# Kernel tuning notes

Measured on AMD Instinct MI355X. Metric: run time of the kernel, lower is better.

The kernel has to match this reference:

```python
import jax, jax.numpy as jnp
import numpy as np

NEG_SLOPE = 0.2
EPS = 1e-6
K = 16


def vec_lna(x, Wf, Wd):
    # x: (B, Cin, 3, ...). Vector-neuron linear + VN-LeakyReLU.
    p = jnp.einsum('oc,bc...->bo...', Wf, x)          # features (B, Cout, 3, ...)
    d = jnp.einsum('oc,bc...->bo...', Wd, x)          # directions (B, Cd, 3, ...), Cd=Cout or 1 (shared)
    dot = jnp.sum(p * d, axis=2, keepdims=True)
    dsq = jnp.sum(d * d, axis=2, keepdims=True)
    p_ref = p - (dot / (dsq + EPS)) * d               # reflect negative part onto hyperplane
    return NEG_SLOPE * p + (1.0 - NEG_SLOPE) * jnp.where(dot >= 0, p, p_ref)


def knn_idx_fn(pts, k):
    # pts: (B, N, 3) -> (B, N, k) indices of k nearest neighbors (incl. self)
    sq = jnp.sum(pts * pts, axis=-1)                  # (B, N)
    d2 = sq[:, :, None] + sq[:, None, :] - 2.0 * jnp.einsum('bnd,bmd->bnm', pts, pts)
    _, idx = jax.lax.top_k(-d2, k)                    # smallest distances
    return idx


def graph_feature(x, idx):
    # x: (B, C, 3, N), idx: (B, N, k) -> (B, 2C, 3, N, k)
    nb = jax.vmap(lambda xb, ib: xb[:, :, ib])(x, idx)  # (B, C, 3, N, k)
    xc = x[..., None]
    return jnp.concatenate([nb - xc, jnp.broadcast_to(xc, nb.shape)], axis=1)


def _winit(key, co, ci):
    return jax.random.normal(key, (co, ci), dtype=jnp.float32) * np.sqrt(2.0 / ci).astype(np.float32)


def setup_inputs() -> dict:
    key = jax.random.key(0)
    ks = jax.random.split(key, 16)
    B, N = 4, 2048
    x = jax.random.normal(ks[0], (B, 3, N), dtype=jnp.float32)
    return {
        'x': x,
        'w1f': _winit(ks[1], 16, 2),   'w1d': _winit(ks[2], 16, 2),
        'w2f': _winit(ks[3], 32, 32),  'w2d': _winit(ks[4], 32, 32),
        'w3f': _winit(ks[5], 64, 64),  'w3d': _winit(ks[6], 64, 64),
        'w4f': _winit(ks[7], 128, 128),'w4d': _winit(ks[8], 128, 128),
        'wcf': _winit(ks[9], 128, 240),'wcd': _winit(ks[10], 1, 240),   # shared nonlinearity -> 1 dir channel
        'wi1f': _winit(ks[11], 128, 256), 'wi1d': _winit(ks[12], 128, 256),
        'wi2f': _winit(ks[13], 256, 128), 'wi2d': _winit(ks[14], 256, 128),
    }


def reference(x, w1f, w1d, w2f, w2d, w3f, w3d, w4f, w4d, wcf, wcd, wi1f, wi1d, wi2f, wi2d):
    # x: (B, 3, N)
    pts = jnp.transpose(x, (0, 2, 1))                 # (B, N, 3)
    idx = knn_idx_fn(pts, K)                          # (B, N, K) -- fixed graph (use_dg=False)
    h = x[:, None]                                    # (B, 1, 3, N)
    h = vec_lna(graph_feature(h, idx), w1f, w1d)
    x1 = h.mean(axis=-1)                              # (B, 16, 3, N)
    h = vec_lna(graph_feature(x1, idx), w2f, w2d)
    x2 = h.mean(axis=-1)                              # (B, 32, 3, N)
    h = vec_lna(graph_feature(x2, idx), w3f, w3d)
    x3 = h.mean(axis=-1)                              # (B, 64, 3, N)
    h = vec_lna(graph_feature(x3, idx), w4f, w4d)
    x4 = h.mean(axis=-1)                              # (B, 128, 3, N)
    xc = vec_lna(jnp.concatenate([x1, x2, x3, x4], axis=1), wcf, wcd)  # (B, 128, 3, N)
    xm = jnp.broadcast_to(xc.mean(axis=-1, keepdims=True), xc.shape)
    xcat = jnp.concatenate([xc, xm], axis=1)          # (B, 256, 3, N)
    x0 = vec_lna(vec_lna(xcat, wi1f, wi1d), wi2f, wi2d)
    inv = jnp.sum(xcat * x0, axis=2)                  # (B, 256, N) rotation-invariant features
    return inv
```

## Files before the change

kernel.cpp:

```cpp
#include <hip/hip_runtime.h>
#include <hip/hip_fp16.h>

#define NPTS  2048
#define BATCH 4
#define NBP   8192
#define MROWS 24576
#define KNN_K 16

typedef short bf16x8 __attribute__((ext_vector_type(8)));
typedef float f32x4  __attribute__((ext_vector_type(4)));

static __device__ __forceinline__ void split_bf16(float a, unsigned short& h, unsigned short& l)
{
    unsigned u = __float_as_uint(a);
    unsigned hr = (u + 0x7FFFu + ((u >> 16) & 1u)) & 0xFFFF0000u;
    h = (unsigned short)(hr >> 16);
    float rem = a - __uint_as_float(hr);
    unsigned v = __float_as_uint(rem);
    l = (unsigned short)((v + 0x7FFFu + ((v >> 16) & 1u)) >> 16);
}

static __device__ __forceinline__ float bf2(unsigned short h, unsigned short l)
{
    return __uint_as_float((unsigned)h << 16) + __uint_as_float((unsigned)l << 16);
}

static __device__ __forceinline__ float lna_scale(float dot, float dsq)
{
    return (dot < 0.f) ? 0.8f * dot * __builtin_amdgcn_rcpf(dsq + 1e-6f) : 0.f;
}

static __device__ __forceinline__ unsigned long long shfl_xor_u64(unsigned long long v, int mask)
{
    unsigned lo = (unsigned)v, hi = (unsigned)(v >> 32);
    lo = (unsigned)__shfl_xor((int)lo, mask, 64);
    hi = (unsigned)__shfl_xor((int)hi, mask, 64);
    return ((unsigned long long)hi << 32) | lo;
}

static __device__ __forceinline__ int xcd_swizzle(int i, int G)
{
    int batch  = (i >> 1) & 3;
    int within = ((i >> 3) << 1) | (i & 1);
    return batch * (G >> 2) + within;
}

static __device__ __forceinline__ float wbig_val(const float* __restrict__ Wf,
                                                 const float* __restrict__ Wd,
                                                 int j, int c, int O, int C)
{
    if (j < 2 * O) {
        int o = j >> 1;
        return (j & 1) ? Wd[o * 2 * C + c] : Wf[o * 2 * C + c];
    }
    int o = (j - 2 * O) >> 1;
    return (j & 1) ? (Wd[o * 2 * C + C + c] - Wd[o * 2 * C + c])
                   : (Wf[o * 2 * C + C + c] - Wf[o * 2 * C + c]);
}

static __device__ __forceinline__ int frag_ix(int r, int c, int RB)
{
    return (((c >> 5) * RB + (r >> 4)) * 64 + ((c >> 3) & 3) * 16 + (r & 15)) * 8 + (c & 7);
}

#define PC0 1572864
#define PC1 (PC0 + 4096)
#define PC2 (PC1 + 8192)
#define PC3 (PC2 + 32768)
#define PC4 (PC3 + 49152)
#define PC5 (PC4 + 65536)
#define PC6 (PC5 + 65536)
#define KNN_BLOCKS (NBP / 4)
#define PREP_BLOCKS (PC6 / 256)

__global__ __launch_bounds__(256) void prep_knn_kernel(
    const float* __restrict__ x, int* __restrict__ idx,
    __half* __restrict__ AH, float* __restrict__ AG,
    const float* __restrict__ w1f, const float* __restrict__ w1d,
    const float* __restrict__ w2f, const float* __restrict__ w2d,
    unsigned short* __restrict__ Wb2h, unsigned short* __restrict__ Wb2l,
    const float* __restrict__ w3f, const float* __restrict__ w3d,
    unsigned short* __restrict__ Wb3h, unsigned short* __restrict__ Wb3l,
    const float* __restrict__ w4f, const float* __restrict__ w4d,
    unsigned short* __restrict__ Wb4h, unsigned short* __restrict__ Wb4l,
    const float* __restrict__ wcf, const float* __restrict__ wcd,
    unsigned short* __restrict__ Wch, unsigned short* __restrict__ Wcl,
    const float* __restrict__ wi1f, const float* __restrict__ wi1d,
    unsigned short* __restrict__ Wi1h, unsigned short* __restrict__ Wi1l,
    const float* __restrict__ wi2f, const float* __restrict__ wi2d,
    unsigned short* __restrict__ Wi2h, unsigned short* __restrict__ Wi2l)
{
    __shared__ unsigned ksh[4][64 * 34];
    if (blockIdx.x < KNN_BLOCKS) {
        const int t  = threadIdx.x & 63;
        const int wq = threadIdx.x >> 6;
        const int bn = blockIdx.x * 4 + wq;
        const int b = bn >> 11;
        const int n = bn & (NPTS - 1);
        const float* xb = x + b * 3 * NPTS;
        const float qx = xb[n], qy = xb[NPTS + n], qz = xb[2 * NPTS + n];
        const float sqn = fmaf(qz, qz, fmaf(qy, qy, qx * qx));
        unsigned* ks = &ksh[wq][t * 34];

        unsigned gm[4];
        int ga[4];
#pragma unroll
        for (int g = 0; g < 4; g++) {
            unsigned kk[8];
#pragma unroll
            for (int j = 0; j < 8; j++) {
                const int i = g * 8 + j;
                const int m = (i << 6) + t;
                float mx = xb[m], my = xb[NPTS + m], mz = xb[2 * NPTS + m];
                float sqm = fmaf(mz, mz, fmaf(my, my, mx * mx));
                float dt  = fmaf(qz, mz, fmaf(qy, my, qx * mx));
                float d2  = sqn + sqm - 2.0f * dt;
                unsigned u = __float_as_uint(d2);
                u ^= (u & 0x80000000u) ? 0xFFFFFFFFu : 0x80000000u;
                kk[j] = u;
            }
            *(uint2*)&ks[g * 8 + 0] = make_uint2(kk[0], kk[1]);
            *(uint2*)&ks[g * 8 + 2] = make_uint2(kk[2], kk[3]);
            *(uint2*)&ks[g * 8 + 4] = make_uint2(kk[4], kk[5]);
            *(uint2*)&ks[g * 8 + 6] = make_uint2(kk[6], kk[7]);
            unsigned bg = kk[0];
            int ba = g * 8;
#pragma unroll
            for (int j = 1; j < 8; j++) {
                if (kk[j] < bg) { bg = kk[j]; ba = g * 8 + j; }
            }
            gm[g] = bg; ga[g] = ba;
        }
        unsigned lm = gm[0];
        int il = ga[0];
#pragma unroll
        for (int g = 1; g < 4; g++) if (gm[g] < lm) { lm = gm[g]; il = ga[g]; }

        unsigned long long pk = ((unsigned long long)lm << 32) | (unsigned)((il << 6) | t);
        int res = -1;
        for (int r = 0; r < KNN_K; r++) {
            unsigned long long w = pk;
#pragma unroll
            for (int off = 32; off > 0; off >>= 1) {
                unsigned long long o = shfl_xor_u64(w, off);
                w = (o < w) ? o : w;
            }
            if (t == r) res = (int)(w & 0xFFFFFFFFull);

            if (pk == w) {
                ks[il] = 0xFFFFFFFFu;
                const int g = il >> 3;
                unsigned bg = ks[g * 8];
                int ba = g * 8;
#pragma unroll
                for (int j = 1; j < 8; j++) {
                    unsigned kv = ks[g * 8 + j];
                    if (kv < bg) { bg = kv; ba = g * 8 + j; }
                }
                gm[g] = bg; ga[g] = ba;
                lm = gm[0]; il = ga[0];
#pragma unroll
                for (int g2 = 1; g2 < 4; g2++) if (gm[g2] < lm) { lm = gm[g2]; il = ga[g2]; }
                pk = ((unsigned long long)lm << 32) | (unsigned)((il << 6) | t);
            }
        }
        if (t < KNN_K) idx[bn * KNN_K + t] = res;
        return;
    }

    const int i = (blockIdx.x - KNN_BLOCKS) * 256 + threadIdx.x;
    if (i < PC0) {
        int o = i & 63;
        int row = i >> 6;
        int v = row % 3;
        int gp = row / 3;
        int b = gp >> 11;
        int n = gp & (NPTS - 1);
        float xv = x[(b * 3 + v) * NPTS + n];
        float wv = wbig_val(w1f, w1d, o, 0, 16, 1);
        float val = xv * wv;
        if (o < 32) AH[(size_t)row * 32 + o] = __float2half(val);
        else        AG[(size_t)row * 32 + o - 32] = val;
    } else if (i < PC6) {
        float v = 0.f;
        unsigned short *ph, *pl;
        int ix;
        if (i < PC1) {
            ix = i - PC0;
            int c = ix & 31, j = ix >> 5;
            if (c < 16) v = wbig_val(w2f, w2d, j, c, 32, 16);
            ph = Wb2h; pl = Wb2l;
        } else if (i < PC2) {
            ix = i - PC1;
            int c = ix & 31, j = ix >> 5;
            v = wbig_val(w3f, w3d, j, c, 64, 32);
            ph = Wb3h; pl = Wb3l;
        } else if (i < PC3) {
            ix = i - PC2;
            int c = ix & 63, j = ix >> 6;
            v = wbig_val(w4f, w4d, j, c, 128, 64);
            ph = Wb4h; pl = Wb4l;
        } else if (i < PC4) {
            ix = i - PC3;
            int c = ix & 255, r = ix >> 8;
            if (c < 240) {
                if (r < 128) v = wcf[r * 240 + c];
                else if (r < 129) v = wcd[(r - 128) * 240 + c];
            }
            ph = Wch; pl = Wcl;
            ix = frag_ix(r, c, 12);
        } else if (i < PC5) {
            ix = i - PC4;
            int c = ix & 255, r = ix >> 8;
            if (r < 128) v = wi1f[r * 256 + c];
            else v = wi1d[(r - 128) * 256 + c];
            ph = Wi1h; pl = Wi1l;
        } else {
            ix = i - PC5;
            int c = ix & 127, r = ix >> 7;
            int o = r >> 1;
            v = (r & 1) ? wi2d[o * 128 + c] : wi2f[o * 128 + c];
            ph = Wi2h; pl = Wi2l;
            ix = frag_ix(r, c, 32);
        }
        unsigned short h, l;
        split_bf16(v, h, l);
        ph[ix] = h; pl[ix] = l;
    }
}

template <int OIN, int NF>
__global__ __launch_bounds__(256, 3) void edge_gemm_kernel(
    const __half* __restrict__ AHin, const float* __restrict__ AGin,
    const int* __restrict__ idx,
    unsigned short* __restrict__ X240h, unsigned short* __restrict__ X240l, int ooff,
    const unsigned short* __restrict__ Wh, const unsigned short* __restrict__ Wl,
    __half* __restrict__ OUTA, float* __restrict__ OUTG)
{
    constexpr int PTS = 16;
    constexpr int NC = NF * 64;
    constexpr int twoO = NC / 2;
    constexpr int LDW = 40;
    constexpr int CPT = OIN / 16;
    constexpr int twoOin = 2 * OIN;

    __shared__ unsigned short Xsh[48][32];
    __shared__ unsigned short Xsl[48][32];
    __shared__ unsigned short wbh[NC][LDW];
    __shared__ unsigned short wbl[NC][LDW];
    __shared__ int sIdx[PTS][KNN_K];

    const int lb = xcd_swizzle(blockIdx.x, gridDim.x);
    const int tid = threadIdx.x;

    for (int rr = tid; rr < NC; rr += 256) {
#pragma unroll
        for (int scc = 0; scc < 4; scc++) {
            *(uint4*)&wbh[rr][scc * 8] = *(const uint4*)(Wh + (size_t)rr * 32 + scc * 8);
            *(uint4*)&wbl[rr][scc * 8] = *(const uint4*)(Wl + (size_t)rr * 32 + scc * 8);
        }
    }
    for (int j = tid; j < PTS * KNN_K; j += 256)
        sIdx[j >> 4][j & 15] = idx[(lb * PTS + (j >> 4)) * KNN_K + (j & 15)];
    __syncthreads();

    const int op = tid & 15;
    const int pt = tid >> 4;
    const int gp = lb * PTS + pt;
    const int b = gp >> 11;
    const int rown = gp * 3;
    const int bbase = (b << 11) * 3;

    float cg[3][2 * CPT];
#pragma unroll
    for (int v = 0; v < 3; v++) {
        if constexpr (CPT == 2) {
            float4 c4 = *(const float4*)&AGin[(size_t)(rown + v) * twoOin + 4 * op];
            cg[v][0] = c4.x; cg[v][1] = c4.y; cg[v][2] = c4.z; cg[v][3] = c4.w;
        } else {
            float2 c2 = *(const float2*)&AGin[(size_t)(rown + v) * twoOin + 2 * op];
            cg[v][0] = c2.x; cg[v][1] = c2.y;
        }
    }
    float am[CPT][3];
#pragma unroll
    for (int c0 = 0; c0 < CPT; c0++) { am[c0][0] = 0.f; am[c0][1] = 0.f; am[c0][2] = 0.f; }

#pragma unroll 2
    for (int k = 0; k < KNN_K; k++) {
        const int m = sIdx[pt][k];
        const __half* base = AHin + (size_t)(bbase + m * 3) * twoOin + 2 * CPT * op;
        float e[3][2 * CPT];
#pragma unroll
        for (int v = 0; v < 3; v++) {
            if constexpr (CPT == 2) {
                uint2 u = *(const uint2*)(base + (size_t)v * twoOin);
                float2 x0 = __half22float2(*(__half2*)&u.x);
                float2 x1 = __half22float2(*(__half2*)&u.y);
                e[v][0] = x0.x; e[v][1] = x0.y; e[v][2] = x1.x; e[v][3] = x1.y;
            } else {
                unsigned u = *(const unsigned*)(base + (size_t)v * twoOin);
                float2 x0 = __half22float2(*(__half2*)&u);
                e[v][0] = x0.x; e[v][1] = x0.y;
            }
        }
#pragma unroll
        for (int c0 = 0; c0 < CPT; c0++) {
            float p0 = e[0][2 * c0] + cg[0][2 * c0], d0 = e[0][2 * c0 + 1] + cg[0][2 * c0 + 1];
            float p1 = e[1][2 * c0] + cg[1][2 * c0], d1 = e[1][2 * c0 + 1] + cg[1][2 * c0 + 1];
            float p2 = e[2][2 * c0] + cg[2][2 * c0], d2 = e[2][2 * c0 + 1] + cg[2][2 * c0 + 1];
            float dot = fmaf(p2, d2, fmaf(p1, d1, p0 * d0));
            float dsq = fmaf(d2, d2, fmaf(d1, d1, d0 * d0));
            float s = lna_scale(dot, dsq);
            am[c0][0] += fmaf(-s, d0, p0);
            am[c0][1] += fmaf(-s, d1, p1);
            am[c0][2] += fmaf(-s, d2, p2);
        }
    }

#pragma unroll
    for (int v = 0; v < 3; v++) {
#pragma unroll
        for (int c0 = 0; c0 < CPT; c0++) {
            const int ch = CPT * op + c0;
            unsigned short h, l;
            split_bf16(am[c0][v] * 0.0625f, h, l);
            Xsh[pt * 3 + v][ch] = h;
            Xsl[pt * 3 + v][ch] = l;
            const size_t ob = (size_t)(rown + v) * 256 + ooff + ch;
            X240h[ob] = h; X240l[ob] = l;
        }
        if constexpr (CPT == 1) {
            Xsh[pt * 3 + v][16 + op] = 0;
            Xsl[pt * 3 + v][16 + op] = 0;
        }
    }
    __syncthreads();

    const int lane = tid & 63;
    const int wv = tid >> 6;
    const int mr = lane & 15;
    const int q  = lane >> 4;

    f32x4 acc[3][NF];
#pragma unroll
    for (int a = 0; a < 3; a++)
#pragma unroll
        for (int c = 0; c < NF; c++) acc[a][c] = (f32x4){0.f, 0.f, 0.f, 0.f};

    bf16x8 ah[3], al[3], bh[NF], bl[NF];
#pragma unroll
    for (int mf = 0; mf < 3; mf++) {
        ah[mf] = *(const bf16x8*)&Xsh[mf * 16 + mr][q * 8];
        al[mf] = *(const bf16x8*)&Xsl[mf * 16 + mr][q * 8];
    }
#pragma unroll
    for (int nf = 0; nf < NF; nf++) {
        const int wr = wv * 16 * NF + nf * 16 + mr;
        bh[nf] = *(const bf16x8*)&wbh[wr][q * 8];
        bl[nf] = *(const bf16x8*)&wbl[wr][q * 8];
    }
#pragma unroll
    for (int mf = 0; mf < 3; mf++)
#pragma unroll
        for (int nf = 0; nf < NF; nf++) {
            acc[mf][nf] = __builtin_amdgcn_mfma_f32_16x16x32_bf16(ah[mf], bh[nf], acc[mf][nf], 0, 0, 0);
            acc[mf][nf] = __builtin_amdgcn_mfma_f32_16x16x32_bf16(ah[mf], bl[nf], acc[mf][nf], 0, 0, 0);
            acc[mf][nf] = __builtin_amdgcn_mfma_f32_16x16x32_bf16(al[mf], bh[nf], acc[mf][nf], 0, 0, 0);
        }

    const int rbase = lb * 48;
#pragma unroll
    for (int nf = 0; nf < NF; nf++) {
        const int col = wv * 16 * NF + nf * 16 + mr;
#pragma unroll
        for (int mf = 0; mf < 3; mf++)
#pragma unroll
            for (int i = 0; i < 4; i++) {
                const int row = rbase + mf * 16 + q * 4 + i;
                const float val = acc[mf][nf][i];
                if (col < twoO) OUTA[(size_t)row * twoO + col] = __float2half(val);
                else            OUTG[(size_t)row * twoO + col - twoO] = val;
            }
    }
}

__global__ __launch_bounds__(256) void gemm_mfma(
    const unsigned short* __restrict__ Xh, const unsigned short* __restrict__ Xl,
    int ldx, int xoff,
    const unsigned short* __restrict__ Wh, const unsigned short* __restrict__ Wl,
    float* __restrict__ OUT, int ldo, int Nout, int Kpad,
    __half* __restrict__ OUTA, float* __restrict__ OUTG, int twoO)
{
    __shared__ unsigned short Ws[2][64][56];
    const int tid = threadIdx.x;
    const int bm = blockIdx.x * 256;
    const int bo = blockIdx.y * 64;
    const int lane = tid & 63;
    const int wv = tid >> 6;
    const int mr = lane & 15;
    const int q  = lane >> 4;

    f32x4 acc[4][4];
#pragma unroll
    for (int a = 0; a < 4; a++)
#pragma unroll
        for (int c = 0; c < 4; c++) acc[a][c] = (f32x4){0.f, 0.f, 0.f, 0.f};

    const int wr = tid >> 2;
    const int sc = tid & 3;

    for (int k0 = 0; k0 < Kpad; k0 += 32) {
        {
            const uint4 vh = *(const uint4*)(Wh + (size_t)(bo + wr) * Kpad + k0 + sc * 8);
            const uint4 vl = *(const uint4*)(Wl + (size_t)(bo + wr) * Kpad + k0 + sc * 8);
            *(uint4*)&Ws[0][wr][sc * 8] = vh;
            *(uint4*)&Ws[1][wr][sc * 8] = vl;
        }
        __syncthreads();

        bf16x8 ah[4], al[4], bh[4], bl[4];
#pragma unroll
        for (int mf = 0; mf < 4; mf++) {
            const size_t xrow = (size_t)(bm + wv * 64 + mf * 16 + mr) * ldx + xoff + k0 + q * 8;
            ah[mf] = *(const bf16x8*)(Xh + xrow);
            al[mf] = *(const bf16x8*)(Xl + xrow);
        }
#pragma unroll
        for (int nf = 0; nf < 4; nf++) {
            bh[nf] = *(const bf16x8*)&Ws[0][nf * 16 + mr][q * 8];
            bl[nf] = *(const bf16x8*)&Ws[1][nf * 16 + mr][q * 8];
        }
#pragma unroll
        for (int mf = 0; mf < 4; mf++)
#pragma unroll
            for (int nf = 0; nf < 4; nf++) {
                acc[mf][nf] = __builtin_amdgcn_mfma_f32_16x16x32_bf16(ah[mf], bh[nf], acc[mf][nf], 0, 0, 0);
                acc[mf][nf] = __builtin_amdgcn_mfma_f32_16x16x32_bf16(ah[mf], bl[nf], acc[mf][nf], 0, 0, 0);
                acc[mf][nf] = __builtin_amdgcn_mfma_f32_16x16x32_bf16(al[mf], bh[nf], acc[mf][nf], 0, 0, 0);
            }
        __syncthreads();
    }

    if (OUTA) {
#pragma unroll
        for (int nf = 0; nf < 4; nf++) {
            const int col = bo + nf * 16 + mr;
            if (col < twoO) {
#pragma unroll
                for (int mf = 0; mf < 4; mf++)
#pragma unroll
                    for (int i = 0; i < 4; i++) {
                        const int row = bm + wv * 64 + mf * 16 + q * 4 + i;
                        OUTA[(size_t)row * twoO + col] = __float2half(acc[mf][nf][i]);
                    }
            } else {
#pragma unroll
                for (int mf = 0; mf < 4; mf++)
#pragma unroll
                    for (int i = 0; i < 4; i++) {
                        const int row = bm + wv * 64 + mf * 16 + q * 4 + i;
                        OUTG[(size_t)row * twoO + col - twoO] = acc[mf][nf][i];
                    }
            }
        }
    } else {
#pragma unroll
        for (int nf = 0; nf < 4; nf++) {
            const int col = bo + nf * 16 + mr;
            if (col < Nout) {
#pragma unroll
                for (int mf = 0; mf < 4; mf++)
#pragma unroll
                    for (int i = 0; i < 4; i++) {
                        const int row = bm + wv * 64 + mf * 16 + q * 4 + i;
                        OUT[(size_t)row * ldo + col] = acc[mf][nf][i];
                    }
            }
        }
    }
}

template <int O, int PT>
__global__ __launch_bounds__(256, 6) void edge_kernel(const __half* __restrict__ AH,
                                                      const float* __restrict__ AG,
                                                      const int* __restrict__ idx,
                                                      unsigned short* __restrict__ outh,
                                                      unsigned short* __restrict__ outl,
                                                      int ooff)
{
    constexpr int TP = O / 2;
    constexpr int twoO = 2 * O;
    const int lb = xcd_swizzle(blockIdx.x, gridDim.x);
    const int tid = threadIdx.x;
    const int op = tid % TP;
    const int pt = tid / TP;
    const int gp = lb * PT + pt;
    const int b = gp >> 11;
    __shared__ int sIdx[PT][KNN_K];
    for (int j = tid; j < PT * KNN_K; j += 256)
        sIdx[j >> 4][j & 15] = idx[(lb * PT + (j >> 4)) * KNN_K + (j & 15)];
    __syncthreads();
    const int rown = gp * 3;
    const float4 c0 = *(const float4*)&AG[(size_t)(rown + 0) * twoO + 4 * op];
    const float4 c1 = *(const float4*)&AG[(size_t)(rown + 1) * twoO + 4 * op];
    const float4 c2 = *(const float4*)&AG[(size_t)(rown + 2) * twoO + 4 * op];
    float ax0 = 0.f, ax1 = 0.f, ax2 = 0.f;
    float ay0 = 0.f, ay1 = 0.f, ay2 = 0.f;
    const int bbase = (b << 11) * 3;
#pragma unroll 2
    for (int k = 0; k < KNN_K; k++) {
        int m = sIdx[pt][k];
        const __half* base = AH + (size_t)(bbase + m * 3) * twoO + 4 * op;
        uint2 u0 = *(const uint2*)(base);
        uint2 u1 = *(const uint2*)(base + twoO);
        uint2 u2 = *(const uint2*)(base + 2 * twoO);
        float2 e0 = __half22float2(*(__half2*)&u0.x);
        float2 f0 = __half22float2(*(__half2*)&u0.y);
        float2 e1 = __half22float2(*(__half2*)&u1.x);
        float2 f1 = __half22float2(*(__half2*)&u1.y);
        float2 e2 = __half22float2(*(__half2*)&u2.x);
        float2 f2 = __half22float2(*(__half2*)&u2.y);
        {
            float p0 = e0.x + c0.x, d0 = e0.y + c0.y;
            float p1 = e1.x + c1.x, d1 = e1.y + c1.y;
            float p2 = e2.x + c2.x, d2 = e2.y + c2.y;
            float dot = fmaf(p2, d2, fmaf(p1, d1, p0 * d0));
            float dsq = fmaf(d2, d2, fmaf(d1, d1, d0 * d0));
            float s = lna_scale(dot, dsq);
            ax0 += fmaf(-s, d0, p0);
            ax1 += fmaf(-s, d1, p1);
            ax2 += fmaf(-s, d2, p2);
        }
        {
            float p0 = f0.x + c0.z, d0 = f0.y + c0.w;
            float p1 = f1.x + c1.z, d1 = f1.y + c1.w;
            float p2 = f2.x + c2.z, d2 = f2.y + c2.w;
            float dot = fmaf(p2, d2, fmaf(p1, d1, p0 * d0));
            float dsq = fmaf(d2, d2, fmaf(d1, d1, d0 * d0));
            float s = lna_scale(dot, dsq);
            ay0 += fmaf(-s, d0, p0);
            ay1 += fmaf(-s, d1, p1);
            ay2 += fmaf(-s, d2, p2);
        }
    }
    float rx[3] = { ax0 * 0.0625f, ax1 * 0.0625f, ax2 * 0.0625f };
    float ry[3] = { ay0 * 0.0625f, ay1 * 0.0625f, ay2 * 0.0625f };
#pragma unroll
    for (int v = 0; v < 3; v++) {
        unsigned short hx, lx, hy, ly;
        split_bf16(rx[v], hx, lx);
        split_bf16(ry[v], hy, ly);
        const size_t ob = (size_t)(rown + v) * 256 + ooff + 2 * op;
        *(unsigned*)(outh + ob) = (unsigned)hx | ((unsigned)hy << 16);
        *(unsigned*)(outl + ob) = (unsigned)lx | ((unsigned)ly << 16);
    }
}

#define EW_LDX 136
#define EW_LDT 133
__global__ __launch_bounds__(256, 4) void edge_wc_kernel(
    const __half* __restrict__ AHin, const float* __restrict__ AGin,
    const int* __restrict__ idx,
    const unsigned short* __restrict__ Xh, const unsigned short* __restrict__ Xl,
    const unsigned short* __restrict__ Wh, const unsigned short* __restrict__ Wl,
    unsigned short* __restrict__ oh, unsigned short* __restrict__ ol,
    float* __restrict__ part2)
{
    __shared__ __align__(16) char smem[48 * EW_LDX * 2 * 2];
    unsigned short (*x4h)[EW_LDX] = (unsigned short (*)[EW_LDX])smem;
    unsigned short (*x4l)[EW_LDX] = (unsigned short (*)[EW_LDX])(smem + 48 * EW_LDX * 2);
    float* tb = (float*)smem;
    __shared__ int sIdx[16][KNN_K];

    const int lb = xcd_swizzle(blockIdx.x, gridDim.x);
    const int tid = threadIdx.x;

    for (int j = tid; j < 16 * KNN_K; j += 256)
        sIdx[j >> 4][j & 15] = idx[(lb * 16 + (j >> 4)) * KNN_K + (j & 15)];
    __syncthreads();

    {
        const int op = tid & 15;
        const int pt = tid >> 4;
        const int gp = lb * 16 + pt;
        const int b = gp >> 11;
        const int rown = gp * 3;
        const int bbase = (b << 11) * 3;

        float cg[3][16];
#pragma unroll
        for (int v = 0; v < 3; v++) {
            const float* ag = &AGin[(size_t)(rown + v) * 256 + 16 * op];
#pragma unroll
            for (int t = 0; t < 4; t++) {
                float4 c4 = *(const float4*)(ag + 4 * t);
                cg[v][4 * t + 0] = c4.x; cg[v][4 * t + 1] = c4.y;
                cg[v][4 * t + 2] = c4.z; cg[v][4 * t + 3] = c4.w;
            }
        }
        float am[8][3];
#pragma unroll
        for (int c0 = 0; c0 < 8; c0++) { am[c0][0] = 0.f; am[c0][1] = 0.f; am[c0][2] = 0.f; }

        for (int k = 0; k < KNN_K; k++) {
            const int m = sIdx[pt][k];
            const __half* base = AHin + (size_t)(bbase + m * 3) * 256 + 16 * op;
            unsigned uw[3][8];
#pragma unroll
            for (int v = 0; v < 3; v++) {
                uint4 a  = *(const uint4*)(base + (size_t)v * 256);
                uint4 bq = *(const uint4*)(base + (size_t)v * 256 + 8);
                uw[v][0] = a.x;  uw[v][1] = a.y;  uw[v][2] = a.z;  uw[v][3] = a.w;
                uw[v][4] = bq.x; uw[v][5] = bq.y; uw[v][6] = bq.z; uw[v][7] = bq.w;
            }
#pragma unroll
            for (int c0 = 0; c0 < 8; c0++) {
                float2 e0 = __half22float2(*(__half2*)&uw[0][c0]);
                float2 e1 = __half22float2(*(__half2*)&uw[1][c0]);
                float2 e2 = __half22float2(*(__half2*)&uw[2][c0]);
                float p0 = e0.x + cg[0][2 * c0], d0 = e0.y + cg[0][2 * c0 + 1];
                float p1 = e1.x + cg[1][2 * c0], d1 = e1.y + cg[1][2 * c0 + 1];
                float p2 = e2.x + cg[2][2 * c0], d2 = e2.y + cg[2][2 * c0 + 1];
                float dot = fmaf(p2, d2, fmaf(p1, d1, p0 * d0));
                float dsq = fmaf(d2, d2, fmaf(d1, d1, d0 * d0));
                float s = lna_scale(dot, dsq);
                am[c0][0] += fmaf(-s, d0, p0);
                am[c0][1] += fmaf(-s, d1, p1);
                am[c0][2] += fmaf(-s, d2, p2);
            }
        }
#pragma unroll
        for (int v = 0; v < 3; v++)
#pragma unroll
            for (int c0 = 0; c0 < 8; c0++) {
                unsigned short h, l;
                split_bf16(am[c0][v] * 0.0625f, h, l);
                x4h[pt * 3 + v][8 * op + c0] = h;
                x4l[pt * 3 + v][8 * op + c0] = l;
            }
    }
    __syncthreads();

    const int lane = tid & 63;
    const int wv = tid >> 6;
    const int mr = lane & 15;
    const int q  = lane >> 4;
    const int rbase = lb * 48;

    f32x4 acc[3][3];
#pragma unroll
    for (int a = 0; a < 3; a++)
#pragma unroll
        for (int c = 0; c < 3; c++) acc[a][c] = (f32x4){0.f, 0.f, 0.f, 0.f};

    for (int k0 = 0; k0 < 256; k0 += 32) {
        const int kb = k0 + q * 8;
        bf16x8 ah[3], al[3], bh[3], bl[3];
#pragma unroll
        for (int mf = 0; mf < 3; mf++) {
            const int row = mf * 16 + mr;
            if (kb >= 112) {
                if (kb >= 240) {
                    ah[mf] = (bf16x8){0, 0, 0, 0, 0, 0, 0, 0};
                    al[mf] = (bf16x8){0, 0, 0, 0, 0, 0, 0, 0};
                } else {
                    ah[mf] = *(const bf16x8*)&x4h[row][kb - 112];
                    al[mf] = *(const bf16x8*)&x4l[row][kb - 112];
                }
            } else {
                const size_t xr = (size_t)(rbase + row) * 256 + kb;
                ah[mf] = *(const bf16x8*)(Xh + xr);
                al[mf] = *(const bf16x8*)(Xl + xr);
            }
        }
#pragma unroll
        for (int nf = 0; nf < 3; nf++) {
            const size_t wri = (size_t)((((k0 >> 5) * 12) + wv * 3 + nf) * 64 + lane) * 8;
            bh[nf] = *(const bf16x8*)(Wh + wri);
            bl[nf] = *(const bf16x8*)(Wl + wri);
        }
#pragma unroll
        for (int mf = 0; mf < 3; mf++)
#pragma unroll
            for (int nf = 0; nf < 3; nf++) {
                acc[mf][nf] = __builtin_amdgcn_mfma_f32_16x16x32_bf16(ah[mf], bh[nf], acc[mf][nf], 0, 0, 0);
                acc[mf][nf] = __builtin_amdgcn_mfma_f32_16x16x32_bf16(ah[mf], bl[nf], acc[mf][nf], 0, 0, 0);
                acc[mf][nf] = __builtin_amdgcn_mfma_f32_16x16x32_bf16(al[mf], bh[nf], acc[mf][nf], 0, 0, 0);
            }
    }
    __syncthreads();

#pragma unroll
    for (int mf = 0; mf < 3; mf++)
#pragma unroll
        for (int nf = 0; nf < 3; nf++) {
            const int col = wv * 48 + nf * 16 + mr;
            if (col <= 128) {
#pragma unroll
                for (int i = 0; i < 4; i++)
                    tb[(mf * 16 + q * 4 + i) * EW_LDT + col] = acc[mf][nf][i];
            }
        }
    __syncthreads();

    const int bp0 = lb * 16;
    float vacc[3] = {0.f, 0.f, 0.f};
#pragma unroll
    for (int it = 0; it < 8; it++) {
        const int item = it * 256 + tid;
        const int o = item & 127;
        const int pt = item >> 7;
        float p[3], d[3];
#pragma unroll
        for (int v = 0; v < 3; v++) {
            const int r = pt * 3 + v;
            p[v] = tb[r * EW_LDT + o];
            d[v] = tb[r * EW_LDT + 128];
        }
        float dot = fmaf(p[2], d[2], fmaf(p[1], d[1], p[0] * d[0]));
        float dsq = fmaf(d[2], d[2], fmaf(d[1], d[1], d[0] * d[0]));
        float s = lna_scale(dot, dsq);
#pragma unroll
        for (int v = 0; v < 3; v++) {
            float val = fmaf(-s, d[v], p[v]);
            vacc[v] += val;
            unsigned short h, l;
            split_bf16(val, h, l);
            const size_t ob = ((size_t)(bp0 + pt) * 3 + v) * 128 + o;
            oh[ob] = h; ol[ob] = l;
        }
    }

    __syncthreads();
    tb[tid] = vacc[0]; tb[256 + tid] = vacc[1]; tb[512 + tid] = vacc[2];
    __syncthreads();
    if (tid < 128) {
#pragma unroll
        for (int v = 0; v < 3; v++)
            part2[(size_t)lb * 384 + v * 128 + tid] =
                tb[v * 256 + tid] + tb[v * 256 + tid + 128];
    }
}

__global__ __launch_bounds__(128) void xm_reduce_ym_kernel(
    const float* __restrict__ part2,
    unsigned short* __restrict__ xmh, unsigned short* __restrict__ xml,
    const float* __restrict__ wi1f, const float* __restrict__ wi1d,
    float* __restrict__ ym)
{
    __shared__ float xs[128];
    const int bv = blockIdx.x;
    const int b = bv / 3;
    const int v = bv % 3;
    const int o = threadIdx.x;
    float acc = 0.f;
    for (int i = 0; i < 128; i++)
        acc += part2[(size_t)(b * 128 + i) * 384 + v * 128 + o];
    const float m = acc * (1.f / 2048.f);
    unsigned short h, l;
    split_bf16(m, h, l);
    xmh[bv * 128 + o] = h;
    xml[bv * 128 + o] = l;
    xs[o] = m;
    __syncthreads();
#pragma unroll
    for (int half = 0; half < 2; half++) {
        const int oo = half * 128 + o;
        const float* wrow = (oo < 128) ? (wi1f + (size_t)oo * 256 + 128)
                                       : (wi1d + (size_t)(oo - 128) * 256 + 128);
        float s = 0.f;
        for (int c = 0; c < 128; c++) s = fmaf(wrow[c], xs[c], s);
        ym[(size_t)bv * 256 + oo] = s;
    }
}

#define QI_LDY  136
#define QI_LDT  257
#define QI_LDT2 67
__global__ __launch_bounds__(256, 2) void gemm_ii_kernel(
    const unsigned short* __restrict__ xch, const unsigned short* __restrict__ xcl,
    const unsigned short* __restrict__ W1h, const unsigned short* __restrict__ W1l,
    const unsigned short* __restrict__ W2h, const unsigned short* __restrict__ W2l,
    const unsigned short* __restrict__ xmh, const unsigned short* __restrict__ xml,
    const float* __restrict__ ym,
    float* __restrict__ out)
{
    __shared__ __align__(16) char regA[51456];
    __shared__ __align__(16) unsigned short y1h[48][QI_LDY];
    __shared__ __align__(16) unsigned short y1l[48][QI_LDY];
    unsigned short* wb = (unsigned short*)regA;
    float* tb = (float*)regA;

    const int tid = threadIdx.x;
    const int lane = tid & 63;
    const int wv = tid >> 6;
    const int mr = lane & 15;
    const int q  = lane >> 4;
    const int lb = blockIdx.x;
    const int bm = lb * 48;
    const int bb = (lb * 16) >> 11;

    f32x4 acc[3][4];
#pragma unroll
    for (int a = 0; a < 3; a++)
#pragma unroll
        for (int c = 0; c < 4; c++) acc[a][c] = (f32x4){0.f, 0.f, 0.f, 0.f};

    for (int k0 = 0; k0 < 128; k0 += 32) {
        {
            const int rr = tid;
#pragma unroll
            for (int sc = 0; sc < 4; sc++) {
                *(uint4*)&wb[(size_t)rr * 40 + sc * 8] =
                    *(const uint4*)(W1h + (size_t)rr * 256 + k0 + sc * 8);
                *(uint4*)&wb[(size_t)(256 + rr) * 40 + sc * 8] =
                    *(const uint4*)(W1l + (size_t)rr * 256 + k0 + sc * 8);
            }
        }
        __syncthreads();

        bf16x8 ah[3], al[3], bh[4], bl[4];
#pragma unroll
        for (int mf = 0; mf < 3; mf++) {
            const size_t xr = (size_t)(bm + mf * 16 + mr) * 128 + k0 + q * 8;
            ah[mf] = *(const bf16x8*)(xch + xr);
            al[mf] = *(const bf16x8*)(xcl + xr);
        }
#pragma unroll
        for (int nf = 0; nf < 4; nf++) {
            const int wr = wv * 64 + nf * 16 + mr;
            bh[nf] = *(const bf16x8*)&wb[(size_t)wr * 40 + q * 8];
            bl[nf] = *(const bf16x8*)&wb[(size_t)(256 + wr) * 40 + q * 8];
        }
#pragma unroll
        for (int mf = 0; mf < 3; mf++)
#pragma unroll
            for (int nf = 0; nf < 4; nf++) {
                acc[mf][nf] = __builtin_amdgcn_mfma_f32_16x16x32_bf16(ah[mf], bh[nf], acc[mf][nf], 0, 0, 0);
                acc[mf][nf] = __builtin_amdgcn_mfma_f32_16x16x32_bf16(ah[mf], bl[nf], acc[mf][nf], 0, 0, 0);
                acc[mf][nf] = __builtin_amdgcn_mfma_f32_16x16x32_bf16(al[mf], bh[nf], acc[mf][nf], 0, 0, 0);
            }
        __syncthreads();
    }

#pragma unroll
    for (int mf = 0; mf < 3; mf++)
#pragma unroll
        for (int nf = 0; nf < 4; nf++)
#pragma unroll
            for (int i = 0; i < 4; i++)
                tb[(size_t)(mf * 16 + q * 4 + i) * QI_LDT + wv * 64 + nf * 16 + mr] = acc[mf][nf][i];
    __syncthreads();

    {
        const int oo = tid & 127;
        float ymp[3], ymd[3];
#pragma unroll
        for (int v = 0; v < 3; v++) {
            ymp[v] = ym[(size_t)(bb * 3 + v) * 256 + oo];
            ymd[v] = ym[(size_t)(bb * 3 + v) * 256 + 128 + oo];
        }
#pragma unroll
        for (int it = 0; it < 8; it++) {
            const int item = it * 256 + tid;
            const int o = item & 127;
            const int pt = item >> 7;
            float p[3], d[3];
#pragma unroll
            for (int v = 0; v < 3; v++) {
                const int r = pt * 3 + v;
                p[v] = tb[(size_t)r * QI_LDT + o] + ymp[v];
                d[v] = tb[(size_t)r * QI_LDT + 128 + o] + ymd[v];
            }
            float dot = fmaf(p[2], d[2], fmaf(p[1], d[1], p[0] * d[0]));
            float dsq = fmaf(d[2], d[2], fmaf(d[1], d[1], d[0] * d[0]));
            float s = lna_scale(dot, dsq);
#pragma unroll
            for (int v = 0; v < 3; v++) {
                unsigned short h, l;
                split_bf16(fmaf(-s, d[v], p[v]), h, l);
                y1h[pt * 3 + v][o] = h;
                y1l[pt * 3 + v][o] = l;
            }
        }
    }
    __syncthreads();

    f32x4 acc2[3][8];
#pragma unroll
    for (int a = 0; a < 3; a++)
#pragma unroll
        for (int c = 0; c < 8; c++) acc2[a][c] = (f32x4){0.f, 0.f, 0.f, 0.f};

    for (int k0 = 0; k0 < 128; k0 += 32) {
        bf16x8 ah[3], al[3];
#pragma unroll
        for (int mf = 0; mf < 3; mf++) {
            ah[mf] = *(const bf16x8*)&y1h[mf * 16 + mr][k0 + q * 8];
            al[mf] = *(const bf16x8*)&y1l[mf * 16 + mr][k0 + q * 8];
        }
#pragma unroll
        for (int nf = 0; nf < 8; nf++) {
            const size_t wi = (size_t)((((k0 >> 5) * 32) + wv * 8 + nf) * 64 + lane) * 8;
            const bf16x8 bh = *(const bf16x8*)(W2h + wi);
            const bf16x8 bl = *(const bf16x8*)(W2l + wi);
#pragma unroll
            for (int mf = 0; mf < 3; mf++) {
                acc2[mf][nf] = __builtin_amdgcn_mfma_f32_16x16x32_bf16(ah[mf], bh, acc2[mf][nf], 0, 0, 0);
                acc2[mf][nf] = __builtin_amdgcn_mfma_f32_16x16x32_bf16(ah[mf], bl, acc2[mf][nf], 0, 0, 0);
                acc2[mf][nf] = __builtin_amdgcn_mfma_f32_16x16x32_bf16(al[mf], bh, acc2[mf][nf], 0, 0, 0);
            }
        }
    }

    float* wt = tb + wv * (48 * QI_LDT2);
#pragma unroll
    for (int hf = 0; hf < 2; hf++) {
        __syncthreads();
#pragma unroll
        for (int mf = 0; mf < 3; mf++)
#pragma unroll
            for (int nf2 = 0; nf2 < 4; nf2++)
#pragma unroll
                for (int i = 0; i < 4; i++)
                    wt[(mf * 16 + q * 4 + i) * QI_LDT2 + nf2 * 16 + mr] = acc2[mf][hf * 4 + nf2][i];
#pragma unroll
        for (int j = 0; j < 8; j++) {
            const int item = j * 64 + lane;
            const int ol = item & 31;
            const int pt = item >> 5;
            const int og = wv * 64 + hf * 32 + ol;
            const int gp = lb * 16 + pt;
            float p[3], d[3], xc[3];
#pragma unroll
            for (int v = 0; v < 3; v++) {
                p[v] = wt[(3 * pt + v) * QI_LDT2 + 2 * ol];
                d[v] = wt[(3 * pt + v) * QI_LDT2 + 2 * ol + 1];
                if (og < 128) {
                    const size_t ix = (size_t)(gp * 3 + v) * 128 + og;
                    xc[v] = bf2(xch[ix], xcl[ix]);
                } else {
                    const size_t ix = (size_t)(bb * 3 + v) * 128 + og - 128;
                    xc[v] = bf2(xmh[ix], xml[ix]);
                }
            }
            float dot = fmaf(p[2], d[2], fmaf(p[1], d[1], p[0] * d[0]));
            float dsq = fmaf(d[2], d[2], fmaf(d[1], d[1], d[0] * d[0]));
            float s = lna_scale(dot, dsq);
            float inv = 0.f;
#pragma unroll
            for (int v = 0; v < 3; v++)
                inv = fmaf(xc[v], fmaf(-s, d[v], p[v]), inv);
            out[((size_t)bb * 256 + og) * NPTS + (gp & (NPTS - 1))] = inv;
        }
    }
}

extern "C" void kernel_launch(void* const* d_in, const int* in_sizes, int n_in,
                              void* d_out, int out_size, void* d_ws, size_t ws_size,
                              hipStream_t stream)
{
    const float* x    = (const float*)d_in[0];
    const float* w1f  = (const float*)d_in[1];
    const float* w1d  = (const float*)d_in[2];
    const float* w2f  = (const float*)d_in[3];
    const float* w2d  = (const float*)d_in[4];
    const float* w3f  = (const float*)d_in[5];
    const float* w3d  = (const float*)d_in[6];
    const float* w4f  = (const float*)d_in[7];
    const float* w4d  = (const float*)d_in[8];
    const float* wcf  = (const float*)d_in[9];
    const float* wcd  = (const float*)d_in[10];
    const float* wi1f = (const float*)d_in[11];
    const float* wi1d = (const float*)d_in[12];
    const float* wi2f = (const float*)d_in[13];
    const float* wi2d = (const float*)d_in[14];
    float* out = (float*)d_out;

    float* F = (float*)d_ws;
    size_t off = 0;
    float* AG = F + off;                          off += (size_t)MROWS * 512;
    __half* AH = (__half*)(F + off);              off += (size_t)MROWS * 128;
    __half* AH2 = (__half*)(F + off);             off += (size_t)MROWS * 128;
    unsigned short* X240h = (unsigned short*)(F + off); off += (size_t)MROWS * 128;
    unsigned short* X240l = (unsigned short*)(F + off); off += (size_t)MROWS * 128;
    unsigned short* xc2h  = (unsigned short*)(F + off); off += (size_t)MROWS * 64;
    unsigned short* xc2l  = (unsigned short*)(F + off); off += (size_t)MROWS * 64;
    unsigned short* Wb2h = (unsigned short*)(F + off); off += 2048;
    unsigned short* Wb2l = (unsigned short*)(F + off); off += 2048;
    unsigned short* Wb3h = (unsigned short*)(F + off); off += 4096;
    unsigned short* Wb3l = (unsigned short*)(F + off); off += 4096;
    unsigned short* Wb4h = (unsigned short*)(F + off); off += 16384;
    unsigned short* Wb4l = (unsigned short*)(F + off); off += 16384;
    unsigned short* Wch  = (unsigned short*)(F + off); off += 24576;
    unsigned short* Wcl  = (unsigned short*)(F + off); off += 24576;
    unsigned short* Wi1h = (unsigned short*)(F + off); off += 32768;
    unsigned short* Wi1l = (unsigned short*)(F + off); off += 32768;
    unsigned short* Wi2h = (unsigned short*)(F + off); off += 32768;
    unsigned short* Wi2l = (unsigned short*)(F + off); off += 32768;
    float* part2 = F + off;                       off += (size_t)512 * 384;
    float* ym    = F + off;                       off += 12 * 256;
    unsigned short* xmph = (unsigned short*)(F + off); off += 768;
    unsigned short* xmpl = (unsigned short*)(F + off); off += 768;
    int* idx    = (int*)(F + off);                off += NBP * KNN_K;
    float* AG2 = AG + (size_t)MROWS * 256;

    prep_knn_kernel<<<KNN_BLOCKS + PREP_BLOCKS, 256, 0, stream>>>(
        x, idx, AH, AG, w1f, w1d,
        w2f, w2d, Wb2h, Wb2l, w3f, w3d, Wb3h, Wb3l, w4f, w4d, Wb4h, Wb4l,
        wcf, wcd, Wch, Wcl, wi1f, wi1d, Wi1h, Wi1l, wi2f, wi2d, Wi2h, Wi2l);

    const int GM = MROWS / 256;

    edge_gemm_kernel<16, 2><<<NBP / 16, 256, 0, stream>>>(
        AH, AG, idx, X240h, X240l, 0, Wb2h, Wb2l, AH2, AG2);
    edge_gemm_kernel<32, 4><<<NBP / 16, 256, 0, stream>>>(
        AH2, AG2, idx, X240h, X240l, 16, Wb3h, Wb3l, AH, AG);
    edge_kernel<64, 8><<<NBP / 8, 256, 0, stream>>>(AH, AG, idx, X240h, X240l, 48);
    gemm_mfma<<<dim3(GM, 8), 256, 0, stream>>>(X240h, X240l, 256, 48, Wb4h, Wb4l, nullptr, 0, 512, 64, AH2, AG2, 256);

    edge_wc_kernel<<<NBP / 16, 256, 0, stream>>>(AH2, AG2, idx, X240h, X240l,
                                                 Wch, Wcl, xc2h, xc2l, part2);

    xm_reduce_ym_kernel<<<BATCH * 3, 128, 0, stream>>>(part2, xmph, xmpl, wi1f, wi1d, ym);

    gemm_ii_kernel<<<MROWS / 48, 256, 0, stream>>>(xc2h, xc2l, Wi1h, Wi1l,
                                                   Wi2h, Wi2l, xmph, xmpl, ym, out);

    (void)in_sizes; (void)n_in; (void)out_size; (void)ws_size;
}
```

Baseline: 256.7 us.

## Pad point rows to four so MFMA accumulators hold full xyz vectors

The final two-layer invariant GEMM kernel now pads each point's three vector rows to four, so one MFMA 16x16 accumulator lane holds p and d for a whole point. The epilogues then run directly from registers, with no LDS transpose. W1 is pre-packed into fragment layout and read straight from global memory instead of being staged through LDS, and W2 is reordered so feature and direction blocks are separate. LDS use drops, which permits 3 blocks per CU, but a quarter of the MFMA work is wasted on zero padding rows.

```diff
diff --git a/kernel.cpp b/kernel.cpp
--- a/kernel.cpp
+++ b/kernel.cpp
@@ -68,7 +68,7 @@
 #define PC2 (PC1 + 8192)
 #define PC3 (PC2 + 32768)
 #define PC4 (PC3 + 49152)
-#define PC5 (PC4 + 65536)
+#define PC5 (PC4 + 32768)
 #define PC6 (PC5 + 65536)
 #define KNN_BLOCKS (NBP / 4)
 #define PREP_BLOCKS (PC6 / 256)
@@ -211,15 +211,16 @@
             ix = frag_ix(r, c, 12);
         } else if (i < PC5) {
             ix = i - PC4;
-            int c = ix & 255, r = ix >> 8;
+            int c = ix & 127, r = ix >> 7;
             if (r < 128) v = wi1f[r * 256 + c];
             else v = wi1d[(r - 128) * 256 + c];
             ph = Wi1h; pl = Wi1l;
+            ix = frag_ix(r, c, 16);
         } else {
             ix = i - PC5;
             int c = ix & 127, r = ix >> 7;
-            int o = r >> 1;
-            v = (r & 1) ? wi2d[o * 128 + c] : wi2f[o * 128 + c];
+            if (r < 256) v = wi2f[r * 128 + c];
+            else v = wi2d[(r - 256) * 128 + c];
             ph = Wi2h; pl = Wi2l;
             ix = frag_ix(r, c, 32);
         }
@@ -775,10 +776,8 @@
     }
 }
 
-#define QI_LDY  136
-#define QI_LDT  257
-#define QI_LDT2 67
-__global__ __launch_bounds__(256, 2) void gemm_ii_kernel(
+#define QI_LDY 136
+__global__ __launch_bounds__(256, 3) void gemm_ii_kernel(
     const unsigned short* __restrict__ xch, const unsigned short* __restrict__ xcl,
     const unsigned short* __restrict__ W1h, const unsigned short* __restrict__ W1l,
     const unsigned short* __restrict__ W2h, const unsigned short* __restrict__ W2l,
@@ -786,11 +785,8 @@
     const float* __restrict__ ym,
     float* __restrict__ out)
 {
-    __shared__ __align__(16) char regA[51456];
-    __shared__ __align__(16) unsigned short y1h[48][QI_LDY];
-    __shared__ __align__(16) unsigned short y1l[48][QI_LDY];
-    unsigned short* wb = (unsigned short*)regA;
-    float* tb = (float*)regA;
+    __shared__ __align__(16) unsigned short y1h[64][QI_LDY];
+    __shared__ __align__(16) unsigned short y1l[64][QI_LDY];
 
     const int tid = threadIdx.x;
     const int lane = tid & 63;
@@ -798,80 +794,57 @@
     const int mr = lane & 15;
     const int q  = lane >> 4;
     const int lb = blockIdx.x;
-    const int bm = lb * 48;
-    const int bb = (lb * 16) >> 11;
-
-    f32x4 acc[3][4];
-#pragma unroll
-    for (int a = 0; a < 3; a++)
+    const int bp0 = lb * 16;
+    const int bb = bp0 >> 11;
+
+    f32x4 acc[4][4];
+#pragma unroll
+    for (int a = 0; a < 4; a++)
 #pragma unroll
         for (int c = 0; c < 4; c++) acc[a][c] = (f32x4){0.f, 0.f, 0.f, 0.f};
 
     for (int k0 = 0; k0 < 128; k0 += 32) {
-        {
-            const int rr = tid;
-#pragma unroll
-            for (int sc = 0; sc < 4; sc++) {
-                *(uint4*)&wb[(size_t)rr * 40 + sc * 8] =
-                    *(const uint4*)(W1h + (size_t)rr * 256 + k0 + sc * 8);
-                *(uint4*)&wb[(size_t)(256 + rr) * 40 + sc * 8] =
-                    *(const uint4*)(W1l + (size_t)rr * 256 + k0 + sc * 8);
-            }
-        }
-        __syncthreads();
-
-        bf16x8 ah[3], al[3], bh[4], bl[4];
-#pragma unroll
-        for (int mf = 0; mf < 3; mf++) {
-            const size_t xr = (size_t)(bm + mf * 16 + mr) * 128 + k0 + q * 8;
-            ah[mf] = *(const bf16x8*)(xch + xr);
-            al[mf] = *(const bf16x8*)(xcl + xr);
-        }
+        bf16x8 ah[4], al[4];
+#pragma unroll
+        for (int mf = 0; mf < 4; mf++) {
+            const int mrow = mf * 16 + mr;
+            const int pt = mrow >> 2, v = mrow & 3;
+            if (v < 3) {
+                const size_t xr = (size_t)((bp0 + pt) * 3 + v) * 128 + k0 + q * 8;
+                ah[mf] = *(const bf16x8*)(xch + xr);
+                al[mf] = *(const bf16x8*)(xcl + xr);
+            } else {
+                ah[mf] = (bf16x8){0, 0, 0, 0, 0, 0, 0, 0};
+                al[mf] = (bf16x8){0, 0, 0, 0, 0, 0, 0, 0};
+            }
+        }
+        const int ks = k0 >> 5;
 #pragma unroll
         for (int nf = 0; nf < 4; nf++) {
-            const int wr = wv * 64 + nf * 16 + mr;
-            bh[nf] = *(const bf16x8*)&wb[(size_t)wr * 40 + q * 8];
-            bl[nf] = *(const bf16x8*)&wb[(size_t)(256 + wr) * 40 + q * 8];
-        }
-#pragma unroll
-        for (int mf = 0; mf < 3; mf++)
-#pragma unroll
-            for (int nf = 0; nf < 4; nf++) {
-                acc[mf][nf] = __builtin_amdgcn_mfma_f32_16x16x32_bf16(ah[mf], bh[nf], acc[mf][nf], 0, 0, 0);
-                acc[mf][nf] = __builtin_amdgcn_mfma_f32_16x16x32_bf16(ah[mf], bl[nf], acc[mf][nf], 0, 0, 0);
-                acc[mf][nf] = __builtin_amdgcn_mfma_f32_16x16x32_bf16(al[mf], bh[nf], acc[mf][nf], 0, 0, 0);
-            }
-        __syncthreads();
-    }
-
-#pragma unroll
-    for (int mf = 0; mf < 3; mf++)
-#pragma unroll
-        for (int nf = 0; nf < 4; nf++)
-#pragma unroll
-            for (int i = 0; i < 4; i++)
-                tb[(size_t)(mf * 16 + q * 4 + i) * QI_LDT + wv * 64 + nf * 16 + mr] = acc[mf][nf][i];
-    __syncthreads();
-
-    {
-        const int oo = tid & 127;
-        float ymp[3], ymd[3];
-#pragma unroll
-        for (int v = 0; v < 3; v++) {
-            ymp[v] = ym[(size_t)(bb * 3 + v) * 256 + oo];
-            ymd[v] = ym[(size_t)(bb * 3 + v) * 256 + 128 + oo];
-        }
-#pragma unroll
-        for (int it = 0; it < 8; it++) {
-            const int item = it * 256 + tid;
-            const int o = item & 127;
-            const int pt = item >> 7;
+            const int rbI = (nf < 2) ? (wv * 2 + nf) : (8 + wv * 2 + (nf - 2));
+            const size_t wi = (size_t)((ks * 16 + rbI) * 64 + lane) * 8;
+            const bf16x8 bh = *(const bf16x8*)(W1h + wi);
+            const bf16x8 bl = *(const bf16x8*)(W1l + wi);
+#pragma unroll
+            for (int mf = 0; mf < 4; mf++) {
+                acc[mf][nf] = __builtin_amdgcn_mfma_f32_16x16x32_bf16(ah[mf], bh, acc[mf][nf], 0, 0, 0);
+                acc[mf][nf] = __builtin_amdgcn_mfma_f32_16x16x32_bf16(ah[mf], bl, acc[mf][nf], 0, 0, 0);
+                acc[mf][nf] = __builtin_amdgcn_mfma_f32_16x16x32_bf16(al[mf], bh, acc[mf][nf], 0, 0, 0);
+            }
+        }
+    }
+
+#pragma unroll
+    for (int mf = 0; mf < 4; mf++) {
+        const int pt = mf * 4 + q;
+#pragma unroll
+        for (int nfp = 0; nfp < 2; nfp++) {
+            const int o = wv * 32 + nfp * 16 + mr;
             float p[3], d[3];
 #pragma unroll
             for (int v = 0; v < 3; v++) {
-                const int r = pt * 3 + v;
-                p[v] = tb[(size_t)r * QI_LDT + o] + ymp[v];
-                d[v] = tb[(size_t)r * QI_LDT + 128 + o] + ymd[v];
+                p[v] = acc[mf][nfp][v]     + ym[(size_t)(bb * 3 + v) * 256 + o];
+                d[v] = acc[mf][nfp + 2][v] + ym[(size_t)(bb * 3 + v) * 256 + 128 + o];
             }
             float dot = fmaf(p[2], d[2], fmaf(p[1], d[1], p[0] * d[0]));
             float dsq = fmaf(d[2], d[2], fmaf(d[1], d[1], d[0] * d[0]));
@@ -880,79 +853,84 @@
             for (int v = 0; v < 3; v++) {
                 unsigned short h, l;
                 split_bf16(fmaf(-s, d[v], p[v]), h, l);
-                y1h[pt * 3 + v][o] = h;
-                y1l[pt * 3 + v][o] = l;
-            }
+                y1h[pt * 4 + v][o] = h;
+                y1l[pt * 4 + v][o] = l;
+            }
+            y1h[pt * 4 + 3][o] = 0;
+            y1l[pt * 4 + 3][o] = 0;
         }
     }
     __syncthreads();
 
-    f32x4 acc2[3][8];
-#pragma unroll
-    for (int a = 0; a < 3; a++)
-#pragma unroll
-        for (int c = 0; c < 8; c++) acc2[a][c] = (f32x4){0.f, 0.f, 0.f, 0.f};
-
-    for (int k0 = 0; k0 < 128; k0 += 32) {
-        bf16x8 ah[3], al[3];
-#pragma unroll
-        for (int mf = 0; mf < 3; mf++) {
-            ah[mf] = *(const bf16x8*)&y1h[mf * 16 + mr][k0 + q * 8];
-            al[mf] = *(const bf16x8*)&y1l[mf * 16 + mr][k0 + q * 8];
-        }
-#pragma unroll
-        for (int nf = 0; nf < 8; nf++) {
-            const size_t wi = (size_t)((((k0 >> 5) * 32) + wv * 8 + nf) * 64 + lane) * 8;
-            const bf16x8 bh = *(const bf16x8*)(W2h + wi);
-            const bf16x8 bl = *(const bf16x8*)(W2l + wi);
-#pragma unroll
-            for (int mf = 0; mf < 3; mf++) {
-                acc2[mf][nf] = __builtin_amdgcn_mfma_f32_16x16x32_bf16(ah[mf], bh, acc2[mf][nf], 0, 0, 0);
-                acc2[mf][nf] = __builtin_amdgcn_mfma_f32_16x16x32_bf16(ah[mf], bl, acc2[mf][nf], 0, 0, 0);
-                acc2[mf][nf] = __builtin_amdgcn_mfma_f32_16x16x32_bf16(al[mf], bh, acc2[mf][nf], 0, 0, 0);
-            }
-        }
-    }
-
-    float* wt = tb + wv * (48 * QI_LDT2);
-#pragma unroll
-    for (int hf = 0; hf < 2; hf++) {
-        __syncthreads();
-#pragma unroll
-        for (int mf = 0; mf < 3; mf++)
-#pragma unroll
-            for (int nf2 = 0; nf2 < 4; nf2++)
-#pragma unroll
-                for (int i = 0; i < 4; i++)
-                    wt[(mf * 16 + q * 4 + i) * QI_LDT2 + nf2 * 16 + mr] = acc2[mf][hf * 4 + nf2][i];
-#pragma unroll
-        for (int j = 0; j < 8; j++) {
-            const int item = j * 64 + lane;
-            const int ol = item & 31;
-            const int pt = item >> 5;
-            const int og = wv * 64 + hf * 32 + ol;
-            const int gp = lb * 16 + pt;
-            float p[3], d[3], xc[3];
-#pragma unroll
-            for (int v = 0; v < 3; v++) {
-                p[v] = wt[(3 * pt + v) * QI_LDT2 + 2 * ol];
-                d[v] = wt[(3 * pt + v) * QI_LDT2 + 2 * ol + 1];
-                if (og < 128) {
-                    const size_t ix = (size_t)(gp * 3 + v) * 128 + og;
-                    xc[v] = bf2(xch[ix], xcl[ix]);
-                } else {
-                    const size_t ix = (size_t)(bb * 3 + v) * 128 + og - 128;
-                    xc[v] = bf2(xmh[ix], xml[ix]);
+    for (int half = 0; half < 2; half++) {
+        f32x4 accp[4][2], accd[4][2];
+#pragma unroll
+        for (int a = 0; a < 4; a++)
+#pragma unroll
+            for (int c = 0; c < 2; c++) {
+                accp[a][c] = (f32x4){0.f, 0.f, 0.f, 0.f};
+                accd[a][c] = (f32x4){0.f, 0.f, 0.f, 0.f};
+            }
+
+        for (int k0 = 0; k0 < 128; k0 += 32) {
+            bf16x8 ah[4], al[4];
+#pragma unroll
+            for (int mf = 0; mf < 4; mf++) {
+                ah[mf] = *(const bf16x8*)&y1h[mf * 16 + mr][k0 + q * 8];
+                al[mf] = *(const bf16x8*)&y1l[mf * 16 + mr][k0 + q * 8];
+            }
+            const int ks = k0 >> 5;
+#pragma unroll
+            for (int nf2 = 0; nf2 < 2; nf2++) {
+                const int rb = wv * 4 + half * 2 + nf2;
+                const size_t wip = (size_t)((ks * 32 + rb) * 64 + lane) * 8;
+                const size_t wid = (size_t)((ks * 32 + 16 + rb) * 64 + lane) * 8;
+                const bf16x8 bph = *(const bf16x8*)(W2h + wip);
+                const bf16x8 bpl = *(const bf16x8*)(W2l + wip);
+                const bf16x8 bdh = *(const bf16x8*)(W2h + wid);
+                const bf16x8 bdl = *(const bf16x8*)(W2l + wid);
+#pragma unroll
+                for (int mf = 0; mf < 4; mf++) {
+                    accp[mf][nf2] = __builtin_amdgcn_mfma_f32_16x16x32_bf16(ah[mf], bph, accp[mf][nf2], 0, 0, 0);
+                    accp[mf][nf2] = __builtin_amdgcn_mfma_f32_16x16x32_bf16(ah[mf], bpl, accp[mf][nf2], 0, 0, 0);
+                    accp[mf][nf2] = __builtin_amdgcn_mfma_f32_16x16x32_bf16(al[mf], bph, accp[mf][nf2], 0, 0, 0);
+                    accd[mf][nf2] = __builtin_amdgcn_mfma_f32_16x16x32_bf16(ah[mf], bdh, accd[mf][nf2], 0, 0, 0);
+                    accd[mf][nf2] = __builtin_amdgcn_mfma_f32_16x16x32_bf16(ah[mf], bdl, accd[mf][nf2], 0, 0, 0);
+                    accd[mf][nf2] = __builtin_amdgcn_mfma_f32_16x16x32_bf16(al[mf], bdh, accd[mf][nf2], 0, 0, 0);
                 }
             }
-            float dot = fmaf(p[2], d[2], fmaf(p[1], d[1], p[0] * d[0]));
-            float dsq = fmaf(d[2], d[2], fmaf(d[1], d[1], d[0] * d[0]));
-            float s = lna_scale(dot, dsq);
-            float inv = 0.f;
-#pragma unroll
-            for (int v = 0; v < 3; v++)
-                inv = fmaf(xc[v], fmaf(-s, d[v], p[v]), inv);
-            out[((size_t)bb * 256 + og) * NPTS + (gp & (NPTS - 1))] = inv;
+        }
+
+#pragma unroll
+        for (int mf = 0; mf < 4; mf++) {
+            const int pt = mf * 4 + q;
+            const int gp = bp0 + pt;
+            const int n = gp & (NPTS - 1);
+#pragma unroll
+            for (int nf2 = 0; nf2 < 2; nf2++) {
+                const int o = wv * 64 + half * 32 + nf2 * 16 + mr;
+                float p[3], d[3], xc[3];
+#pragma unroll
+                for (int v = 0; v < 3; v++) {
+                    p[v] = accp[mf][nf2][v];
+                    d[v] = accd[mf][nf2][v];
+                    if (o < 128) {
+                        const size_t ix = (size_t)(gp * 3 + v) * 128 + o;
+                        xc[v] = bf2(xch[ix], xcl[ix]);
+                    } else {
+                        const size_t ix = (size_t)(bb * 3 + v) * 128 + o - 128;
+                        xc[v] = bf2(xmh[ix], xml[ix]);
+                    }
+                }
+                float dot = fmaf(p[2], d[2], fmaf(p[1], d[1], p[0] * d[0]));
+                float dsq = fmaf(d[2], d[2], fmaf(d[1], d[1], d[0] * d[0]));
+                float s = lna_scale(dot, dsq);
+                float inv = 0.f;
+#pragma unroll
+                for (int v = 0; v < 3; v++)
+                    inv = fmaf(xc[v], fmaf(-s, d[v], p[v]), inv);
+                out[((size_t)bb * 256 + o) * NPTS + n] = inv;
+            }
         }
     }
 }
```

After: 283.3 us. 10.4% more time.
